# Kernel optimization log

Measured on AMD Instinct MI355X. Metric: run time of the kernel, lower is better.

## Reference

```python
import jax, jax.numpy as jnp
import numpy as np

H = 3584        # hidden_size
NH = 16         # num_attention_heads
HD = 256        # head_dim
NKV = 8         # num_key_value_heads
GROUPS = NH // NKV
B, S = 2, 2048
SOFTCAP = 50.0
SCALE = 256.0 ** -0.5   # query_pre_attn_scalar ** -0.5
ROPE_BASE = 10000.0
NEG = -1e9


def _rotate_half(x):
    x1, x2 = jnp.split(x, 2, axis=-1)
    return jnp.concatenate([-x2, x1], axis=-1)


def _apply_rope(x, cos, sin):
    # x: [b, h, s, d]; cos/sin: [s, d]
    return x * cos[None, None] + _rotate_half(x) * sin[None, None]


def setup_inputs() -> dict:
    key = jax.random.key(0)
    k1, k2, k3, k4, k5 = jax.random.split(key, 5)
    hidden_states = jax.random.normal(k1, (B, S, H), dtype=jnp.float32)
    # additive causal mask [1, 1, S, S]
    causal = jnp.tril(jnp.ones((S, S), dtype=bool))
    attention_mask = jnp.where(causal, 0.0, NEG).astype(jnp.float32)[None, None]
    Wq = jax.random.normal(k2, (H, NH * HD), dtype=jnp.float32) * 0.02
    Wk = jax.random.normal(k3, (H, NKV * HD), dtype=jnp.float32) * 0.02
    Wv = jax.random.normal(k4, (H, NKV * HD), dtype=jnp.float32) * 0.02
    Wo = jax.random.normal(k5, (NH * HD, H), dtype=jnp.float32) * 0.02
    return {"hidden_states": hidden_states, "attention_mask": attention_mask,
            "Wq": Wq, "Wk": Wk, "Wv": Wv, "Wo": Wo}


def reference(hidden_states, attention_mask, Wq, Wk, Wv, Wo):
    b, s, _ = hidden_states.shape
    q = (hidden_states @ Wq).reshape(b, s, NH, HD).transpose(0, 2, 1, 3)   # [b,nh,s,d]
    k = (hidden_states @ Wk).reshape(b, s, NKV, HD).transpose(0, 2, 1, 3)  # [b,nkv,s,d]
    v = (hidden_states @ Wv).reshape(b, s, NKV, HD).transpose(0, 2, 1, 3)

    # RoPE (HF-style: freqs duplicated, rotate_half)
    pos = jnp.arange(s, dtype=jnp.float32)
    inv_freq = 1.0 / (ROPE_BASE ** (jnp.arange(0, HD, 2, dtype=jnp.float32) / HD))
    freqs = pos[:, None] * inv_freq[None, :]          # [s, d/2]
    emb = jnp.concatenate([freqs, freqs], axis=-1)    # [s, d]
    cos, sin = jnp.cos(emb), jnp.sin(emb)
    q = _apply_rope(q, cos, sin)
    k = _apply_rope(k, cos, sin)

    # repeat_kv for GQA
    k = jnp.repeat(k, GROUPS, axis=1)  # [b,nh,s,d]
    v = jnp.repeat(v, GROUPS, axis=1)

    scores = jnp.einsum('bhsd,bhtd->bhst', q, k) * SCALE
    # tanh logit softcapping
    scores = jnp.tanh(scores / SOFTCAP) * SOFTCAP
    scores = scores + attention_mask
    probs = jax.nn.softmax(scores.astype(jnp.float32), axis=-1).astype(q.dtype)
    out = jnp.einsum('bhst,bhtd->bhsd', probs, v)
    out = out.transpose(0, 2, 1, 3).reshape(b, s, NH * HD)
    return out @ Wo
```

## Files before the change

kernel.cpp:

```cpp
#include <hip/hip_runtime.h>
#include <cstdint>
#include <cstddef>

typedef __bf16 bf16x8 __attribute__((ext_vector_type(8)));
typedef unsigned short u16x8 __attribute__((ext_vector_type(8)));
typedef float  f32x4  __attribute__((ext_vector_type(4)));
typedef unsigned short u16;

#define GLDS16(GP, LP) __builtin_amdgcn_global_load_lds( \
    (const __attribute__((address_space(1))) void*)(GP), \
    (__attribute__((address_space(3))) void*)(LP), 16, 0, 0)

__device__ __forceinline__ float b2f(u16 u) {
  unsigned int x = ((unsigned int)u) << 16;
  return __builtin_bit_cast(float, x);
}
__device__ __forceinline__ u16 f2b(float f) {
  unsigned int u = __builtin_bit_cast(unsigned int, f);
  unsigned int r = (u + 0x7fffu + ((u >> 16) & 1u)) >> 16;
  return (u16)r;
}

constexpr int Bc  = 2;
constexpr int Sc  = 2048;
constexpr int Hc  = 3584;
constexpr int NHc = 16;
constexpr int HDc = 256;
constexpr int NKV = 8;
constexpr int QD  = NHc * HDc;
constexpr int QS  = 8192;
constexpr float SCALE   = 0.0625f;
constexpr float CAP     = 50.0f;
constexpr float INV_CAP = 1.0f / 50.0f;

__device__ __forceinline__ float softcap(float raw) {
  float e = __expf(raw * (2.0f * SCALE * INV_CAP));
  return CAP - (2.0f * CAP) * __builtin_amdgcn_rcpf(1.0f + e);
}

__global__ void rope_table_k(float* __restrict__ cosT, float* __restrict__ sinT) {
  int idx = blockIdx.x * 256 + threadIdx.x;
  int s = idx >> 7, i = idx & 127;
  float inv = expf((float)i * -0.0719557841560639f);
  float ang = (float)s * inv;
  cosT[idx] = cosf(ang);
  sinT[idx] = sinf(ang);
}

__global__ void cvt_f32_bf16(const float4* __restrict__ in, ushort4* __restrict__ out, int n4) {
  int i = blockIdx.x * 256 + threadIdx.x;
  int st = gridDim.x * 256;
  for (; i < n4; i += st) {
    float4 v = in[i];
    ushort4 u;
    u.x = f2b(v.x); u.y = f2b(v.y); u.z = f2b(v.z); u.w = f2b(v.w);
    out[i] = u;
  }
}

__global__ void transpose_cvt(const float* __restrict__ in, u16* __restrict__ out, int R, int C) {
  __shared__ float t[32][33];
  int c0 = blockIdx.x * 32, r0 = blockIdx.y * 32;
  int tx = threadIdx.x, ty = threadIdx.y;
#pragma unroll
  for (int i = 0; i < 4; i++)
    t[ty + i * 8][tx] = in[(size_t)(r0 + ty + i * 8) * C + c0 + tx];
  __syncthreads();
#pragma unroll
  for (int i = 0; i < 4; i++)
    out[(size_t)(c0 + ty + i * 8) * R + r0 + tx] = f2b(t[tx][ty + i * 8]);
}

__global__ void transpose_v(const u16* __restrict__ QKV, u16* __restrict__ Vt) {
  __shared__ u16 t[32][33];
  int b = blockIdx.z >> 3, kvh = blockIdx.z & 7;
  int s0 = blockIdx.x * 32, d0 = blockIdx.y * 32;
  int tx = threadIdx.x, ty = threadIdx.y;
#pragma unroll
  for (int i = 0; i < 4; i++)
    t[ty + i * 8][tx] = QKV[(size_t)(b * Sc + s0 + ty + i * 8) * QS + 6144 + kvh * HDc + d0 + tx];
  __syncthreads();
#pragma unroll
  for (int i = 0; i < 4; i++)
    Vt[(size_t)((b * NKV + kvh) * HDc + d0 + ty + i * 8) * Sc + s0 + tx] = t[tx][ty + i * 8];
}

template <int NH>
__global__ void rope_apply(u16* __restrict__ X, const float* __restrict__ cosT,
                           const float* __restrict__ sinT) {
  constexpr int LS = (NH == 16) ? 4 : 3;
  int idx = blockIdx.x * 256 + threadIdx.x;
  const int i4 = (idx & 31) << 2;
  const int h = (idx >> 5) & (NH - 1);
  const int row = idx >> (5 + LS);
  const int s = row & (Sc - 1);
  u16* p = X + (size_t)row * QS + h * 256 + i4;
  ushort4 lo = *(const ushort4*)p;
  ushort4 hi = *(const ushort4*)(p + 128);
  float4 c = *(const float4*)(cosT + s * 128 + i4);
  float4 sn = *(const float4*)(sinT + s * 128 + i4);
  ushort4 nlo, nhi;
  { float xl = b2f(lo.x), xh = b2f(hi.x);
    nlo.x = f2b(xl * c.x - xh * sn.x); nhi.x = f2b(xh * c.x + xl * sn.x); }
  { float xl = b2f(lo.y), xh = b2f(hi.y);
    nlo.y = f2b(xl * c.y - xh * sn.y); nhi.y = f2b(xh * c.y + xl * sn.y); }
  { float xl = b2f(lo.z), xh = b2f(hi.z);
    nlo.z = f2b(xl * c.z - xh * sn.z); nhi.z = f2b(xh * c.z + xl * sn.z); }
  { float xl = b2f(lo.w), xh = b2f(hi.w);
    nlo.w = f2b(xl * c.w - xh * sn.w); nhi.w = f2b(xh * c.w + xl * sn.w); }
  *(ushort4*)p = nlo;
  *(ushort4*)(p + 128) = nhi;
}

template <typename OT>
__global__ __launch_bounds__(512, 1) void gemm256(const u16* __restrict__ A,
                                                  const u16* __restrict__ Bt,
                                                  OT* __restrict__ C,
                                                  int M, int N, int K, int GM) {
  __shared__ alignas(16) u16 As[2][256 * 64];
  __shared__ alignas(16) u16 Bs[2][256 * 64];
  const int nwg = gridDim.x;
  const int cpx = nwg >> 3;
  const int wgid = (blockIdx.x & 7) * cpx + (blockIdx.x >> 3);
  const int GN = nwg / GM;
  const int width = 8 * GN;
  const int grp = wgid / width;
  const int rem = wgid - grp * width;
  const int m0 = (grp * 8 + (rem & 7)) * 256;
  const int n0 = (rem >> 3) * 256;
  const int tid = threadIdx.x;
  const int lane = tid & 63;
  const int w = tid >> 6;
  const int wm = w >> 2, wn = w & 3;
  const int lg = lane >> 4, lr = lane & 15;
  const int nkt = K >> 6;

  auto STAGE = [&](int buf, int kt) {
    const int k0 = kt * 64;
#pragma unroll
    for (int i = 0; i < 4; i++) {
      int c = i * 512 + tid;
      int row = c >> 3, slot = c & 7;
      GLDS16(A + (size_t)(m0 + row) * K + k0 + (slot ^ (row & 7)) * 8,
             (char*)As[buf] + c * 16);
    }
#pragma unroll
    for (int i = 0; i < 4; i++) {
      int c = i * 512 + tid;
      int row = c >> 3, slot = c & 7;
      GLDS16(Bt + (size_t)(n0 + row) * K + k0 + (slot ^ (row & 7)) * 8,
             (char*)Bs[buf] + c * 16);
    }
  };

  f32x4 acc[8][4] = {};

  STAGE(0, 0);
  STAGE(1, 1);
  asm volatile("s_waitcnt vmcnt(8)" ::: "memory");
  __builtin_amdgcn_sched_barrier(0);
  __builtin_amdgcn_s_barrier();

  for (int kt = 0; kt < nkt; ++kt) {
    const int buf = kt & 1;
    bf16x8 bfr[4][2], af[4][2], af2[4][2];
#pragma unroll
    for (int j = 0; j < 4; j++)
#pragma unroll
      for (int ks = 0; ks < 2; ks++) {
        int row = wn * 64 + j * 16 + lr;
        bfr[j][ks] = *(const bf16x8*)&Bs[buf][row * 64 + ((ks * 4 + lg) ^ (row & 7)) * 8];
      }
#pragma unroll
    for (int i = 0; i < 4; i++)
#pragma unroll
      for (int ks = 0; ks < 2; ks++) {
        int row = wm * 128 + i * 16 + lr;
        af[i][ks] = *(const bf16x8*)&As[buf][row * 64 + ((ks * 4 + lg) ^ (row & 7)) * 8];
      }
#pragma unroll
    for (int i = 0; i < 4; i++)
#pragma unroll
      for (int ks = 0; ks < 2; ks++) {
        int row = wm * 128 + 64 + i * 16 + lr;
        af2[i][ks] = *(const bf16x8*)&As[buf][row * 64 + ((ks * 4 + lg) ^ (row & 7)) * 8];
      }
    __builtin_amdgcn_s_setprio(1);
#pragma unroll
    for (int i = 0; i < 4; i++)
#pragma unroll
      for (int j = 0; j < 4; j++)
#pragma unroll
        for (int ks = 0; ks < 2; ks++)
          acc[i][j] = __builtin_amdgcn_mfma_f32_16x16x32_bf16(
              af[i][ks], bfr[j][ks], acc[i][j], 0, 0, 0);
    __builtin_amdgcn_s_setprio(0);
    asm volatile("s_waitcnt vmcnt(0) lgkmcnt(0)" ::: "memory");
    __builtin_amdgcn_sched_barrier(0);
    __builtin_amdgcn_s_barrier();
    if (kt + 2 < nkt) STAGE(buf, kt + 2);
    __builtin_amdgcn_s_setprio(1);
#pragma unroll
    for (int i = 0; i < 4; i++)
#pragma unroll
      for (int j = 0; j < 4; j++)
#pragma unroll
        for (int ks = 0; ks < 2; ks++)
          acc[4 + i][j] = __builtin_amdgcn_mfma_f32_16x16x32_bf16(
              af2[i][ks], bfr[j][ks], acc[4 + i][j], 0, 0, 0);
    __builtin_amdgcn_s_setprio(0);
  }

#pragma unroll
  for (int i = 0; i < 8; i++) {
    const int row = m0 + wm * 128 + i * 16 + lg * 4;
#pragma unroll
    for (int j = 0; j < 4; j++) {
      const int col = n0 + wn * 64 + j * 16 + lr;
#pragma unroll
      for (int r = 0; r < 4; r++) {
        if constexpr (sizeof(OT) == 2)
          C[(size_t)(row + r) * N + col] = f2b(acc[i][j][r]);
        else
          C[(size_t)(row + r) * N + col] = acc[i][j][r];
      }
    }
  }
}

__global__ __launch_bounds__(512) void attn_fwd(const u16* __restrict__ QKV,
                                                const u16* __restrict__ Vt,
                                                const float* __restrict__ cosT,
                                                const float* __restrict__ sinT,
                                                u16* __restrict__ AO) {
  constexpr int KVB = 64;
  __shared__ alignas(16) u16 Ks[2][KVB * 256];
  __shared__ alignas(16) u16 Vs[2][256 * KVB];
  __shared__ alignas(16) u16 Ps[8][16][64];
  const int bx = blockIdx.x, h = blockIdx.y, b = blockIdx.z;
  const int qt = b ? (15 - bx) : bx;
  const int q0 = qt * 128;
  const int kvh = h >> 1;
  const int tid = threadIdx.x, w = tid >> 6, lane = tid & 63;
  const int lg = lane >> 4, lr = lane & 15;
  const int myrow = q0 + w * 16 + lr;

  u16x8 qr[8];
  {
    const u16* qp = QKV + (size_t)(b * Sc + myrow) * QS + h * HDc + lg * 8;
#pragma unroll
    for (int kk = 0; kk < 8; kk++) qr[kk] = *(const u16x8*)(qp + kk * 32);
    const float* ct = cosT + myrow * 128 + lg * 8;
    const float* st = sinT + myrow * 128 + lg * 8;
#pragma unroll
    for (int kk = 0; kk < 4; kk++)
#pragma unroll
      for (int q4 = 0; q4 < 2; q4++) {
        float4 c = *(const float4*)(ct + kk * 32 + q4 * 4);
        float4 s = *(const float4*)(st + kk * 32 + q4 * 4);
#pragma unroll
        for (int e = 0; e < 4; e++) {
          int ei = q4 * 4 + e;
          float cc = (&c.x)[e], ss = (&s.x)[e];
          float lo = b2f(qr[kk][ei]), hi = b2f(qr[kk + 4][ei]);
          qr[kk][ei]     = f2b(lo * cc - hi * ss);
          qr[kk + 4][ei] = f2b(hi * cc + lo * ss);
        }
      }
  }
  bf16x8 qf[8];
#pragma unroll
  for (int kk = 0; kk < 8; kk++) qf[kk] = __builtin_bit_cast(bf16x8, qr[kk]);

  f32x4 o[16] = {};
  float m_r[4], l_r[4];
#pragma unroll
  for (int r = 0; r < 4; r++) { m_r[r] = -1e30f; l_r[r] = 0.0f; }
  const int my_qrow = q0 + w * 16 + lg * 4;
  const int wave_min_row = q0 + w * 16;
  const int wave_max_row = q0 + w * 16 + 15;

  const u16* kbase = QKV + (size_t)(b * Sc) * QS + 4096 + kvh * HDc;
  const u16* vbase = Vt + (size_t)((b * NKV + kvh) * HDc) * Sc;

  auto STAGE = [&](int buf, int t0) {
#pragma unroll
    for (int i = 0; i < 4; i++) {
      int c = i * 512 + tid;
      int row = c >> 5, slot = c & 31;
      GLDS16(kbase + (size_t)(t0 + row) * QS + (slot ^ (row & 7)) * 8,
             (char*)Ks[buf] + c * 16);
    }
#pragma unroll
    for (int i = 0; i < 4; i++) {
      int c = i * 512 + tid;
      int d = c >> 3, slot = c & 7;
      GLDS16(vbase + (size_t)d * Sc + t0 + (slot ^ (d & 7)) * 8,
             (char*)Vs[buf] + c * 16);
    }
  };

  const int nt = 2 * qt + 2;
  int cur = 0;
  STAGE(0, 0);
  for (int ti = 0; ti < nt; ++ti) {
    const int t0 = ti * 64;
    if (ti + 1 < nt) {
      STAGE(cur ^ 1, t0 + 64);
      asm volatile("s_waitcnt vmcnt(8)" ::: "memory");
    } else {
      asm volatile("s_waitcnt vmcnt(0)" ::: "memory");
    }
    __builtin_amdgcn_sched_barrier(0);
    __builtin_amdgcn_s_barrier();

    if (t0 <= wave_max_row) {
      const u16* KsT = Ks[cur];
      const u16* VsT = Vs[cur];

      f32x4 sc[4];
#pragma unroll
      for (int j = 0; j < 4; j++) {
        f32x4 a = {0.f, 0.f, 0.f, 0.f};
        const int row = j * 16 + lr;
#pragma unroll
        for (int kk = 0; kk < 8; kk++) {
          int s0 = (kk * 4 + lg) ^ (lr & 7);
          bf16x8 kf = *(const bf16x8*)&KsT[row * 256 + s0 * 8];
          a = __builtin_amdgcn_mfma_f32_16x16x32_bf16(qf[kk], kf, a, 0, 0, 0);
        }
        sc[j] = a;
      }

      float tmax[4] = {-1e30f, -1e30f, -1e30f, -1e30f};
      if (t0 + 63 > wave_min_row) {
#pragma unroll
        for (int j = 0; j < 4; j++)
#pragma unroll
          for (int r = 0; r < 4; r++) {
            float x = softcap(sc[j][r]);
            if (t0 + j * 16 + lr > my_qrow + r) x = -1e9f;
            sc[j][r] = x;
            tmax[r] = fmaxf(tmax[r], x);
          }
      } else {
#pragma unroll
        for (int j = 0; j < 4; j++)
#pragma unroll
          for (int r = 0; r < 4; r++) {
            float x = softcap(sc[j][r]);
            sc[j][r] = x;
            tmax[r] = fmaxf(tmax[r], x);
          }
      }
#pragma unroll
      for (int xm = 1; xm < 16; xm <<= 1)
#pragma unroll
        for (int r = 0; r < 4; r++) tmax[r] = fmaxf(tmax[r], __shfl_xor(tmax[r], xm, 64));

      bool need = false;
#pragma unroll
      for (int r = 0; r < 4; r++) need |= (tmax[r] > m_r[r] + 8.0f);
      if (__any(need)) {
        float scal[4];
#pragma unroll
        for (int r = 0; r < 4; r++) {
          float mn = fmaxf(m_r[r], tmax[r]);
          scal[r] = __expf(m_r[r] - mn);
          m_r[r] = mn;
          l_r[r] *= scal[r];
        }
#pragma unroll
        for (int df = 0; df < 16; df++)
#pragma unroll
          for (int r = 0; r < 4; r++) o[df][r] *= scal[r];
      }

      float psum[4] = {0.f, 0.f, 0.f, 0.f};
#pragma unroll
      for (int j = 0; j < 4; j++)
#pragma unroll
        for (int r = 0; r < 4; r++) {
          float p = __expf(sc[j][r] - m_r[r]);
          psum[r] += p;
          int q = lg * 4 + r;
          Ps[w][q][(j * 16 + lr) ^ ((q & 7) << 3)] = f2b(p);
        }
#pragma unroll
      for (int xm = 1; xm < 16; xm <<= 1)
#pragma unroll
        for (int r = 0; r < 4; r++) psum[r] += __shfl_xor(psum[r], xm, 64);
#pragma unroll
      for (int r = 0; r < 4; r++) l_r[r] += psum[r];

      bf16x8 pf0 = *(const bf16x8*)&Ps[w][lr][(lg ^ (lr & 7)) * 8];
      bf16x8 pf1 = *(const bf16x8*)&Ps[w][lr][((lg ^ 4) ^ (lr & 7)) * 8];
#pragma unroll
      for (int df = 0; df < 16; df++) {
        const int d = df * 16 + lr;
        int s0 = lg ^ (d & 7);
        int s1 = (4 + lg) ^ (d & 7);
        bf16x8 vf0 = *(const bf16x8*)&VsT[d * KVB + s0 * 8];
        o[df] = __builtin_amdgcn_mfma_f32_16x16x32_bf16(pf0, vf0, o[df], 0, 0, 0);
        bf16x8 vf1 = *(const bf16x8*)&VsT[d * KVB + s1 * 8];
        o[df] = __builtin_amdgcn_mfma_f32_16x16x32_bf16(pf1, vf1, o[df], 0, 0, 0);
      }
    }

    __builtin_amdgcn_s_barrier();
    cur ^= 1;
  }

  float inv_l[4];
#pragma unroll
  for (int r = 0; r < 4; r++) inv_l[r] = 1.0f / l_r[r];
  u16* op = AO + (size_t)(b * Sc + my_qrow) * QD + h * HDc + lr;
#pragma unroll
  for (int df = 0; df < 16; df++)
#pragma unroll
    for (int r = 0; r < 4; r++)
      op[(size_t)r * QD + df * 16] = f2b(o[df][r] * inv_l[r]);
}

extern "C" void kernel_launch(void* const* d_in, const int* in_sizes, int n_in,
                              void* d_out, int out_size, void* d_ws, size_t ws_size,
                              hipStream_t stream) {
  (void)in_sizes; (void)n_in; (void)out_size; (void)ws_size;
  const float* hs = (const float*)d_in[0];
  const float* Wq = (const float*)d_in[2];
  const float* Wk = (const float*)d_in[3];
  const float* Wv = (const float*)d_in[4];
  const float* Wo = (const float*)d_in[5];
  float* out = (float*)d_out;
  char* ws = (char*)d_ws;

  float* cosT = (float*)(ws + 0);
  float* sinT = (float*)(ws + 1048576);
  u16* hsb    = (u16*)(ws + 2097152);
  u16* Wqkvt  = (u16*)(ws + 31457280);
  u16* Wot    = (u16*)(ws + 90177536);
  u16* QKVb   = (u16*)(ws + 119537664);
  u16* Vtr    = hsb;
  u16* AO     = Wqkvt;

  dim3 tb32x8(32, 8);

  rope_table_k<<<1024, 256, 0, stream>>>(cosT, sinT);
  cvt_f32_bf16<<<2048, 256, 0, stream>>>((const float4*)hs, (ushort4*)hsb, (Bc * Sc * Hc) / 4);
  transpose_cvt<<<dim3(QD / 32, Hc / 32), tb32x8, 0, stream>>>(Wq, Wqkvt, Hc, QD);
  transpose_cvt<<<dim3(2048 / 32, Hc / 32), tb32x8, 0, stream>>>(Wk, Wqkvt + (size_t)4096 * Hc, Hc, 2048);
  transpose_cvt<<<dim3(2048 / 32, Hc / 32), tb32x8, 0, stream>>>(Wv, Wqkvt + (size_t)6144 * Hc, Hc, 2048);
  transpose_cvt<<<dim3(Hc / 32, QD / 32), tb32x8, 0, stream>>>(Wo, Wot, QD, Hc);

  gemm256<u16><<<dim3(16 * 32), 512, 0, stream>>>(hsb, Wqkvt, QKVb, Bc * Sc, QS, Hc, 16);

  rope_apply<8><<<4096, 256, 0, stream>>>(QKVb + 4096, cosT, sinT);
  transpose_v<<<dim3(Sc / 32, HDc / 32, Bc * NKV), tb32x8, 0, stream>>>(QKVb, Vtr);

  attn_fwd<<<dim3(16, NHc, Bc), 512, 0, stream>>>(QKVb, Vtr, cosT, sinT, AO);

  gemm256<float><<<dim3(16 * 14), 512, 0, stream>>>(AO, Wot, out, Bc * Sc, Hc, QD, 16);
}
```

Before: 596.2 us.

## Split attention waves across query pairs and KV/head-dim halves

```diff
diff --git a/kernel.cpp b/kernel.cpp
--- a/kernel.cpp
+++ b/kernel.cpp
@@ -236,17 +236,25 @@
   constexpr int KVB = 64;
   __shared__ alignas(16) u16 Ks[2][KVB * 256];
   __shared__ alignas(16) u16 Vs[2][256 * KVB];
-  __shared__ alignas(16) u16 Ps[8][16][64];
+  __shared__ alignas(16) u16 Pl[4][32][64];
+  __shared__ float exm[4][2][2][16];
+  __shared__ float exs[4][2][2][16];
   const int bx = blockIdx.x, h = blockIdx.y, b = blockIdx.z;
   const int qt = b ? (15 - bx) : bx;
   const int q0 = qt * 128;
   const int kvh = h >> 1;
   const int tid = threadIdx.x, w = tid >> 6, lane = tid & 63;
   const int lg = lane >> 4, lr = lane & 15;
-  const int myrow = q0 + w * 16 + lr;
-
-  u16x8 qr[8];
-  {
+  const int wq = w & 3, th = w >> 2;
+  const int toff = th * 32, doff = th * 128;
+  const int rbase = q0 + wq * 32;
+  const int wave_max_row = rbase + 31;
+
+  bf16x8 qf[2][8];
+#pragma unroll
+  for (int g = 0; g < 2; g++) {
+    const int myrow = rbase + g * 16 + lr;
+    u16x8 qr[8];
     const u16* qp = QKV + (size_t)(b * Sc + myrow) * QS + h * HDc + lg * 8;
 #pragma unroll
     for (int kk = 0; kk < 8; kk++) qr[kk] = *(const u16x8*)(qp + kk * 32);
@@ -267,18 +275,16 @@
           qr[kk + 4][ei] = f2b(hi * cc + lo * ss);
         }
       }
+#pragma unroll
+    for (int kk = 0; kk < 8; kk++) qf[g][kk] = __builtin_bit_cast(bf16x8, qr[kk]);
   }
-  bf16x8 qf[8];
-#pragma unroll
-  for (int kk = 0; kk < 8; kk++) qf[kk] = __builtin_bit_cast(bf16x8, qr[kk]);
-
-  f32x4 o[16] = {};
-  float m_r[4], l_r[4];
-#pragma unroll
-  for (int r = 0; r < 4; r++) { m_r[r] = -1e30f; l_r[r] = 0.0f; }
-  const int my_qrow = q0 + w * 16 + lg * 4;
-  const int wave_min_row = q0 + w * 16;
-  const int wave_max_row = q0 + w * 16 + 15;
+
+  f32x4 o[2][8] = {};
+  float m_r[2][4], l_r[2][4];
+#pragma unroll
+  for (int g = 0; g < 2; g++)
+#pragma unroll
+    for (int r = 0; r < 4; r++) { m_r[g][r] = -1e30f; l_r[g][r] = 0.0f; }
 
   const u16* kbase = QKV + (size_t)(b * Sc) * QS + 4096 + kvh * HDc;
   const u16* vbase = Vt + (size_t)((b * NKV + kvh) * HDc) * Sc;
@@ -314,96 +320,156 @@
     __builtin_amdgcn_sched_barrier(0);
     __builtin_amdgcn_s_barrier();
 
-    if (t0 <= wave_max_row) {
-      const u16* KsT = Ks[cur];
-      const u16* VsT = Vs[cur];
-
-      f32x4 sc[4];
-#pragma unroll
-      for (int j = 0; j < 4; j++) {
-        f32x4 a = {0.f, 0.f, 0.f, 0.f};
-        const int row = j * 16 + lr;
+    const bool v0t = (t0 <= wave_max_row);
+    const bool v1t = (t0 + 32 <= wave_max_row);
+    const bool cmp = th ? v1t : v0t;
+    const u16* KsT = Ks[cur];
+    const u16* VsT = Vs[cur];
+
+    float tmax[2][4];
+#pragma unroll
+    for (int g = 0; g < 2; g++)
+#pragma unroll
+      for (int r = 0; r < 4; r++) tmax[g][r] = -1e30f;
+    f32x4 sc[2][2];
+
+    if (cmp) {
+#pragma unroll
+      for (int j = 0; j < 2; j++) {
+        const int row = toff + j * 16 + lr;
+        f32x4 a0 = {0.f, 0.f, 0.f, 0.f}, a1 = {0.f, 0.f, 0.f, 0.f};
 #pragma unroll
         for (int kk = 0; kk < 8; kk++) {
           int s0 = (kk * 4 + lg) ^ (lr & 7);
           bf16x8 kf = *(const bf16x8*)&KsT[row * 256 + s0 * 8];
-          a = __builtin_amdgcn_mfma_f32_16x16x32_bf16(qf[kk], kf, a, 0, 0, 0);
+          a0 = __builtin_amdgcn_mfma_f32_16x16x32_bf16(qf[0][kk], kf, a0, 0, 0, 0);
+          a1 = __builtin_amdgcn_mfma_f32_16x16x32_bf16(qf[1][kk], kf, a1, 0, 0, 0);
         }
-        sc[j] = a;
-      }
-
-      float tmax[4] = {-1e30f, -1e30f, -1e30f, -1e30f};
-      if (t0 + 63 > wave_min_row) {
-#pragma unroll
-        for (int j = 0; j < 4; j++)
+        sc[0][j] = a0; sc[1][j] = a1;
+      }
+      if (t0 + toff + 31 > rbase) {
+#pragma unroll
+        for (int g = 0; g < 2; g++)
+#pragma unroll
+          for (int j = 0; j < 2; j++)
+#pragma unroll
+            for (int r = 0; r < 4; r++) {
+              float x = softcap(sc[g][j][r]);
+              if (t0 + toff + j * 16 + lr > rbase + g * 16 + lg * 4 + r) x = -1e9f;
+              sc[g][j][r] = x;
+              tmax[g][r] = fmaxf(tmax[g][r], x);
+            }
+      } else {
+#pragma unroll
+        for (int g = 0; g < 2; g++)
+#pragma unroll
+          for (int j = 0; j < 2; j++)
+#pragma unroll
+            for (int r = 0; r < 4; r++) {
+              float x = softcap(sc[g][j][r]);
+              sc[g][j][r] = x;
+              tmax[g][r] = fmaxf(tmax[g][r], x);
+            }
+      }
+#pragma unroll
+      for (int xm = 1; xm < 16; xm <<= 1)
+#pragma unroll
+        for (int g = 0; g < 2; g++)
+#pragma unroll
+          for (int r = 0; r < 4; r++)
+            tmax[g][r] = fmaxf(tmax[g][r], __shfl_xor(tmax[g][r], xm, 64));
+    }
+
+    if (lr == 0) {
+#pragma unroll
+      for (int g = 0; g < 2; g++)
+#pragma unroll
+        for (int r = 0; r < 4; r++) exm[wq][th][g][lg * 4 + r] = tmax[g][r];
+    }
+    asm volatile("s_waitcnt lgkmcnt(0)" ::: "memory");
+    __builtin_amdgcn_s_barrier();
+#pragma unroll
+    for (int g = 0; g < 2; g++)
+#pragma unroll
+      for (int r = 0; r < 4; r++)
+        tmax[g][r] = fmaxf(tmax[g][r], exm[wq][th ^ 1][g][lg * 4 + r]);
+
+    bool need = false;
+#pragma unroll
+    for (int g = 0; g < 2; g++)
+#pragma unroll
+      for (int r = 0; r < 4; r++) need |= (tmax[g][r] > m_r[g][r] + 8.0f);
+    if (__any(need)) {
+#pragma unroll
+      for (int g = 0; g < 2; g++)
+#pragma unroll
+        for (int r = 0; r < 4; r++) {
+          float mn = fmaxf(m_r[g][r], tmax[g][r]);
+          float scal = __expf(m_r[g][r] - mn);
+          m_r[g][r] = mn;
+          l_r[g][r] *= scal;
+#pragma unroll
+          for (int df = 0; df < 8; df++) o[g][df][r] *= scal;
+        }
+    }
+
+    float psum[2][4] = {};
+    if (cmp) {
+#pragma unroll
+      for (int g = 0; g < 2; g++)
+#pragma unroll
+        for (int j = 0; j < 2; j++)
 #pragma unroll
           for (int r = 0; r < 4; r++) {
-            float x = softcap(sc[j][r]);
-            if (t0 + j * 16 + lr > my_qrow + r) x = -1e9f;
-            sc[j][r] = x;
-            tmax[r] = fmaxf(tmax[r], x);
+            float p = __expf(sc[g][j][r] - m_r[g][r]);
+            psum[g][r] += p;
+            int q = g * 16 + lg * 4 + r;
+            Pl[wq][q][(toff + j * 16 + lr) ^ ((q & 7) << 3)] = f2b(p);
           }
-      } else {
-#pragma unroll
-        for (int j = 0; j < 4; j++)
-#pragma unroll
-          for (int r = 0; r < 4; r++) {
-            float x = softcap(sc[j][r]);
-            sc[j][r] = x;
-            tmax[r] = fmaxf(tmax[r], x);
-          }
-      }
 #pragma unroll
       for (int xm = 1; xm < 16; xm <<= 1)
 #pragma unroll
-        for (int r = 0; r < 4; r++) tmax[r] = fmaxf(tmax[r], __shfl_xor(tmax[r], xm, 64));
-
-      bool need = false;
-#pragma unroll
-      for (int r = 0; r < 4; r++) need |= (tmax[r] > m_r[r] + 8.0f);
-      if (__any(need)) {
-        float scal[4];
-#pragma unroll
-        for (int r = 0; r < 4; r++) {
-          float mn = fmaxf(m_r[r], tmax[r]);
-          scal[r] = __expf(m_r[r] - mn);
-          m_r[r] = mn;
-          l_r[r] *= scal[r];
-        }
-#pragma unroll
-        for (int df = 0; df < 16; df++)
-#pragma unroll
-          for (int r = 0; r < 4; r++) o[df][r] *= scal[r];
-      }
-
-      float psum[4] = {0.f, 0.f, 0.f, 0.f};
-#pragma unroll
-      for (int j = 0; j < 4; j++)
-#pragma unroll
-        for (int r = 0; r < 4; r++) {
-          float p = __expf(sc[j][r] - m_r[r]);
-          psum[r] += p;
-          int q = lg * 4 + r;
-          Ps[w][q][(j * 16 + lr) ^ ((q & 7) << 3)] = f2b(p);
-        }
-#pragma unroll
-      for (int xm = 1; xm < 16; xm <<= 1)
-#pragma unroll
-        for (int r = 0; r < 4; r++) psum[r] += __shfl_xor(psum[r], xm, 64);
-#pragma unroll
-      for (int r = 0; r < 4; r++) l_r[r] += psum[r];
-
-      bf16x8 pf0 = *(const bf16x8*)&Ps[w][lr][(lg ^ (lr & 7)) * 8];
-      bf16x8 pf1 = *(const bf16x8*)&Ps[w][lr][((lg ^ 4) ^ (lr & 7)) * 8];
-#pragma unroll
-      for (int df = 0; df < 16; df++) {
-        const int d = df * 16 + lr;
-        int s0 = lg ^ (d & 7);
-        int s1 = (4 + lg) ^ (d & 7);
-        bf16x8 vf0 = *(const bf16x8*)&VsT[d * KVB + s0 * 8];
-        o[df] = __builtin_amdgcn_mfma_f32_16x16x32_bf16(pf0, vf0, o[df], 0, 0, 0);
-        bf16x8 vf1 = *(const bf16x8*)&VsT[d * KVB + s1 * 8];
-        o[df] = __builtin_amdgcn_mfma_f32_16x16x32_bf16(pf1, vf1, o[df], 0, 0, 0);
+        for (int g = 0; g < 2; g++)
+#pragma unroll
+          for (int r = 0; r < 4; r++) psum[g][r] += __shfl_xor(psum[g][r], xm, 64);
+    }
+    if (lr == 0) {
+#pragma unroll
+      for (int g = 0; g < 2; g++)
+#pragma unroll
+        for (int r = 0; r < 4; r++) exs[wq][th][g][lg * 4 + r] = psum[g][r];
+    }
+    asm volatile("s_waitcnt lgkmcnt(0)" ::: "memory");
+    __builtin_amdgcn_s_barrier();
+#pragma unroll
+    for (int g = 0; g < 2; g++)
+#pragma unroll
+      for (int r = 0; r < 4; r++)
+        l_r[g][r] += psum[g][r] + exs[wq][th ^ 1][g][lg * 4 + r];
+
+    bf16x8 pf[2][2];
+    if (v0t) {
+#pragma unroll
+      for (int g = 0; g < 2; g++)
+        pf[g][0] = *(const bf16x8*)&Pl[wq][g * 16 + lr][(lg ^ (lr & 7)) * 8];
+    }
+    if (v1t) {
+#pragma unroll
+      for (int g = 0; g < 2; g++)
+        pf[g][1] = *(const bf16x8*)&Pl[wq][g * 16 + lr][((4 + lg) ^ (lr & 7)) * 8];
+    }
+#pragma unroll
+    for (int df = 0; df < 8; df++) {
+      const int d = doff + df * 16 + lr;
+      if (v0t) {
+        bf16x8 vf = *(const bf16x8*)&VsT[d * KVB + (lg ^ (d & 7)) * 8];
+        o[0][df] = __builtin_amdgcn_mfma_f32_16x16x32_bf16(pf[0][0], vf, o[0][df], 0, 0, 0);
+        o[1][df] = __builtin_amdgcn_mfma_f32_16x16x32_bf16(pf[1][0], vf, o[1][df], 0, 0, 0);
+      }
+      if (v1t) {
+        bf16x8 vf = *(const bf16x8*)&VsT[d * KVB + ((4 + lg) ^ (d & 7)) * 8];
+        o[0][df] = __builtin_amdgcn_mfma_f32_16x16x32_bf16(pf[0][1], vf, o[0][df], 0, 0, 0);
+        o[1][df] = __builtin_amdgcn_mfma_f32_16x16x32_bf16(pf[1][1], vf, o[1][df], 0, 0, 0);
       }
     }
 
@@ -411,15 +477,18 @@
     cur ^= 1;
   }
 
-  float inv_l[4];
-#pragma unroll
-  for (int r = 0; r < 4; r++) inv_l[r] = 1.0f / l_r[r];
-  u16* op = AO + (size_t)(b * Sc + my_qrow) * QD + h * HDc + lr;
-#pragma unroll
-  for (int df = 0; df < 16; df++)
-#pragma unroll
-    for (int r = 0; r < 4; r++)
-      op[(size_t)r * QD + df * 16] = f2b(o[df][r] * inv_l[r]);
+#pragma unroll
+  for (int g = 0; g < 2; g++) {
+    float inv_l[4];
+#pragma unroll
+    for (int r = 0; r < 4; r++) inv_l[r] = 1.0f / l_r[g][r];
+    u16* op = AO + (size_t)(b * Sc + rbase + g * 16 + lg * 4) * QD + h * HDc + doff + lr;
+#pragma unroll
+    for (int df = 0; df < 8; df++)
+#pragma unroll
+      for (int r = 0; r < 4; r++)
+        op[(size_t)r * QD + df * 16] = f2b(o[g][df][r] * inv_l[r]);
+  }
 }
 
 extern "C" void kernel_launch(void* const* d_in, const int* in_sizes, int n_in,
```

Measured after the change: 717.0 us. +20.3%, slower.
